# Performance work log

Measured on AMD Instinct MI355X. Metric: run time of the kernel, lower is better.

Reference implementation:

```python
import jax, jax.numpy as jnp
import numpy as np

D, NH, K, FF, S, B = 256, 4, 1024, 1024, 2048, 4  # nhead*d_model must equal key_feature_dim=1024


def _ln(x, g, b, eps=1e-5):
    m = jnp.mean(x, axis=-1, keepdims=True)
    v = jnp.mean((x - m) ** 2, axis=-1, keepdims=True)
    return (x - m) / jnp.sqrt(v + eps) * g + b


def _l2norm(x, eps=1e-12):  # F.normalize(p=2, dim=-1)
    n = jnp.sqrt(jnp.sum(x * x, axis=-1, keepdims=True))
    return x / jnp.maximum(n, eps)


def setup_inputs() -> dict:
    key = jax.random.key(0)
    ks = jax.random.split(key, 16)
    def rn(i, shape, s):
        return jax.random.normal(ks[i], shape, jnp.float32) * jnp.float32(s)
    z = lambda shape: jnp.zeros(shape, jnp.float32)
    o = lambda shape: jnp.ones(shape, jnp.float32)
    return {
        "srcc": jax.random.normal(ks[0], (S, B, D), jnp.float32),
        "memory": jax.random.normal(ks[1], (S, B, D), jnp.float32),
        # per-head RelationUnit weights (stacked over NH heads)
        "WK": rn(2, (NH, K, D), np.sqrt(2.0 / K)),
        "WQ": rn(3, (NH, K, D), np.sqrt(2.0 / K)),
        "WV": rn(4, (NH, D, D), np.sqrt(2.0 / D)),
        "Wt": rn(5, (NH, D, D), np.sqrt(1.0 / D)),   # trans_conv
        # per-head TransNonlinear (extra_nonlinear)
        "e1w": rn(6, (NH, K, D), np.sqrt(1.0 / D)), "e1b": z((NH, K)),
        "e2w": rn(7, (NH, D, K), np.sqrt(1.0 / K)), "e2b": z((NH, D)),
        "eg": o((NH, D)), "eb": z((NH, D)),
        "Wout": rn(8, (D, NH * D), np.sqrt(1.0 / (NH * D))),  # trans_conv_out
        # decoder-layer FFN + norms
        "l1w": rn(9, (FF, D), np.sqrt(1.0 / D)), "l1b": z((FF,)),
        "l2w": rn(10, (D, FF), np.sqrt(1.0 / FF)), "l2b": z((D,)),
        "n1g": o((D,)), "n1b": z((D,)),
        "n3g": o((D,)), "n3b": z((D,)),
    }


def _forward(srcc, memory, WK, WQ, WV, Wt, e1w, e1b, e2w, e2b, eg, eb,
             Wout, l1w, l1b, l2w, l2b, n1g, n1b, n3g, n3b):
    # RMA(query=memory, key=srcc, value=srcc); dropout = identity (eval mode)
    q, kv = memory, srcc  # [S,B,D]
    wk = _l2norm(jnp.einsum('sbd,hkd->hsbk', kv, WK))   # [h,S,B,K]
    wq = _l2norm(jnp.einsum('sbd,hkd->hsbk', q, WQ))
    dot = jnp.einsum('hqbk,hsbk->hbqs', wq, wk)          # [h,B,Sq,Sk]
    aff = jax.nn.softmax(dot, axis=-1)
    # custom renormalization over the *query* axis (torch dim=1 of [B,Sq,Sk])
    aff = aff / (1e-9 + jnp.sum(aff, axis=2, keepdims=True))
    wv = jnp.einsum('sbd,hed->hbse', kv, WV)             # [h,B,Sk,D]
    o = jnp.einsum('hbqs,hbse->hqbe', aff, wv)           # [h,Sq,B,D]
    ru = jax.nn.relu(jnp.einsum('hqbd,hed->hqbe', q[None] - o, Wt))
    # per-head TransNonlinear
    hmid = jax.nn.relu(jnp.einsum('hqbd,hkd->hqbk', ru, e1w) + e1b[:, None, None, :])
    s2 = jnp.einsum('hqbk,hdk->hqbd', hmid, e2w) + e2b[:, None, None, :]
    xh = _ln(ru + s2, eg[:, None, None, :], eb[:, None, None, :])  # [h,S,B,D]
    cat = jnp.moveaxis(xh, 0, 2).reshape(q.shape[0], q.shape[1], NH * D)  # concat heads
    rma_out = jnp.einsum('sbk,dk->sbd', cat, Wout)       # [S,B,D]
    # decoder layer: note the faithful `[0]` indexing from the source
    srcc2 = rma_out[0]                                    # [B,D]
    x = _ln(memory + srcc2[None, :, :], n1g, n1b)         # broadcast residual
    ff = jax.nn.relu(x @ l1w.T + l1b) @ l2w.T + l2b
    return _ln(x + ff, n3g, n3b)


def reference(srcc, memory, WK, WQ, WV, Wt, e1w, e1b, e2w, e2b, eg, eb,
              Wout, l1w, l1b, l2w, l2b, n1g, n1b, n3g, n3b):
    return _forward(srcc, memory, WK, WQ, WV, Wt, e1w, e1b, e2w, e2b, eg, eb,
                    Wout, l1w, l1b, l2w, l2b, n1g, n1b, n3g, n3b)
```

## Files before the change

### kernel.cpp

```cpp
#include <hip/hip_runtime.h>
#include <stdint.h>
#include <stdio.h>

#define S_  2048
#define B_  4
#define D_  256
#define NH_ 4
#define K_  1024
#define FF_ 1024
#define M_  (S_*B_)
#define HB_ (NH_*B_)

#define LDSROW 136
#define PROW 144

typedef float  f32x4  __attribute__((ext_vector_type(4)));
typedef float  f32x2  __attribute__((ext_vector_type(2)));
typedef __bf16 bf16x8 __attribute__((ext_vector_type(8)));

__device__ __forceinline__ float bf2f(unsigned short u) {
  union { unsigned int i; float f; } v; v.i = ((unsigned int)u) << 16; return v.f;
}
__device__ __forceinline__ unsigned short f2bf(float f) {
  union { float f; unsigned int i; } v; v.f = f;
  unsigned int r = v.i + 0x7fffu + ((v.i >> 16) & 1u);
  return (unsigned short)(r >> 16);
}
__device__ __forceinline__ unsigned char f2fp8(float f) {
  return (unsigned char)(__builtin_amdgcn_cvt_pk_fp8_f32(f, f, 0, false) & 0xff);
}

__device__ __forceinline__ int kperm(int k) {
  int ks = k >> 5, quad = (k >> 3) & 3, b = k & 7;
  return ((ks >> 1) << 6) + (quad << 4) + ((ks & 1) << 3) + b;
}

__device__ __forceinline__ void gld_lds16(const void* g, void* l) {
  __builtin_amdgcn_global_load_lds(
      (__attribute__((address_space(1))) void*)(uintptr_t)g,
      (__attribute__((address_space(3))) void*)(uintptr_t)l, 16, 0, 0);
}

__device__ __forceinline__ void gemm_kloop(
    const unsigned short* __restrict__ Ag, const unsigned short* __restrict__ Bg,
    int lda, int ldb, int kdim,
    unsigned short* __restrict__ smA, unsigned short* __restrict__ smB,
    f32x4 acc[4][4])
{
  const int t    = threadIdx.x;
  const int wave = t >> 6;
  const int lane = t & 63;
  const int wm   = (wave >> 1) << 6;
  const int wn   = (wave & 1) << 6;
  const int c16  = lane & 15;
  const int quad = lane >> 4;

  for (int kc = 0; kc < kdim; kc += 64) {
    __syncthreads();
#pragma unroll
    for (int it = 0; it < 4; ++it) {
      int c   = it*256 + t;
      int row = c >> 3;
      int g   = (c & 7) ^ (row & 7);
      const unsigned short* ga = Ag + (size_t)row*lda + kc + g*8;
      const unsigned short* gb = Bg + (size_t)row*ldb + kc + g*8;
      unsigned short* la = smA + (size_t)(it*256 + wave*64)*8;
      unsigned short* lb = smB + (size_t)(it*256 + wave*64)*8;
      gld_lds16(ga, la);
      gld_lds16(gb, lb);
    }
    asm volatile("s_waitcnt vmcnt(0)" ::: "memory");
    __syncthreads();
#pragma unroll
    for (int ks = 0; ks < 2; ++ks) {
      bf16x8 av[4], bv[4];
#pragma unroll
      for (int i = 0; i < 4; ++i) {
        int ra = wm + i*16 + c16;
        av[i] = *(const bf16x8*)(smA + ra*64 + (((ks*4 + quad) ^ (ra & 7)))*8);
        int rb = wn + i*16 + c16;
        bv[i] = *(const bf16x8*)(smB + rb*64 + (((ks*4 + quad) ^ (rb & 7)))*8);
      }
#pragma unroll
      for (int i = 0; i < 4; ++i)
#pragma unroll
        for (int j = 0; j < 4; ++j)
          acc[i][j] = __builtin_amdgcn_mfma_f32_16x16x32_bf16(av[i], bv[j], acc[i][j], 0, 0, 0);
    }
  }
}

__device__ __forceinline__ float blk_sum256(float v, float* red) {
#pragma unroll
  for (int o = 32; o; o >>= 1) v += __shfl_xor(v, o, 64);
  __syncthreads();
  if ((threadIdx.x & 63) == 0) red[threadIdx.x >> 6] = v;
  __syncthreads();
  return red[0] + red[1] + red[2] + red[3];
}

__device__ __forceinline__ float wave_red(float a) {
#pragma unroll
  for (int o = 1; o < 64; o <<= 1) a += __shfl_xor(a, o, 64);
  return a;
}

__global__ void __launch_bounds__(256) k_cvt6z(
    const float* __restrict__ s0, unsigned short* __restrict__ d0,
    const float* __restrict__ s1, unsigned short* __restrict__ d1,
    const float* __restrict__ s2, unsigned short* __restrict__ d2,
    const float* __restrict__ s3, unsigned short* __restrict__ d3,
    const float* __restrict__ s4, unsigned short* __restrict__ d4,
    const float* __restrict__ s5, unsigned short* __restrict__ d5,
    float* __restrict__ zbase, int zfloats) {
  int b = blockIdx.x;
  if (b >= 6656) {
    int i = ((b - 6656)*256 + threadIdx.x)*4;
    if (i + 3 < zfloats) *(float4*)(zbase + i) = float4{0.f,0.f,0.f,0.f};
    return;
  }
  const float* src; unsigned short* dst; int base;
  if      (b < 2048) { src = s0; dst = d0; base = b; }
  else if (b < 4096) { src = s1; dst = d1; base = b - 2048; }
  else if (b < 5120) { src = s2; dst = d2; base = b - 4096; }
  else if (b < 6144) { src = s3; dst = d3; base = b - 5120; }
  else if (b < 6400) { src = s4; dst = d4; base = b - 6144; }
  else               { src = s5; dst = d5; base = b - 6400; }
  int i = (base*256 + threadIdx.x)*4;
  float4 v = *(const float4*)(src + i);
  ushort4 o;
  o.x = f2bf(v.x); o.y = f2bf(v.y); o.z = f2bf(v.z); o.w = f2bf(v.w);
  *(ushort4*)(dst + i) = o;
}

__global__ void __launch_bounds__(256) k_proj2(
    const unsigned short* __restrict__ X0, const unsigned short* __restrict__ W0,
    float* __restrict__ n0p, unsigned char* __restrict__ o0p,
    const unsigned short* __restrict__ X1, const unsigned short* __restrict__ W1,
    float* __restrict__ n1p, unsigned char* __restrict__ o1p) {
  __shared__ __align__(16) unsigned char smbuf[32768];
  unsigned short* sm = (unsigned short*)smbuf;
  int which = blockIdx.x >> 11;
  const unsigned short* X = which ? X1 : X0;
  const unsigned short* W = which ? W1 : W0;
  float* nsq = which ? n1p : n0p;
  unsigned char* outp = which ? o1p : o0p;
  int l = blockIdx.x & 2047, x = l & 7, rblk = l >> 3;
  int m0 = (rblk >> 2)*128;
  int n0 = (x*4 + (rblk & 3))*128;
  f32x4 acc[4][4];
#pragma unroll
  for (int i = 0; i < 4; ++i)
#pragma unroll
    for (int j = 0; j < 4; ++j) acc[i][j] = f32x4{0.f,0.f,0.f,0.f};
  gemm_kloop(X + (size_t)m0*D_, W + (size_t)n0*D_, D_, D_, D_, sm, sm + 128*64, acc);
  const int t = threadIdx.x, wave = t>>6, lane = t&63;
  const int wm = (wave>>1)*64, wn = (wave&1)*64, quad = lane>>4, c16 = lane&15;
  const int h = n0 >> 10;
  unsigned char* sm8 = smbuf;
  __syncthreads();
#pragma unroll
  for (int i = 0; i < 4; ++i)
#pragma unroll
    for (int r = 0; r < 4; ++r) {
      int mloc = wm + i*16 + quad*4 + r;
      float sq = 0.f;
#pragma unroll
      for (int j = 0; j < 4; ++j) {
        float v = acc[i][j][r];
        sm8[mloc*PROW + kperm(wn + j*16 + c16)] = f2fp8(v);
        sq += v*v;
      }
      sq += __shfl_xor(sq, 1, 64); sq += __shfl_xor(sq, 2, 64);
      sq += __shfl_xor(sq, 4, 64); sq += __shfl_xor(sq, 8, 64);
      if (c16 == 0) {
        int m = m0 + mloc;
        atomicAdd(&nsq[(size_t)(h*B_ + (m & 3))*S_ + (m >> 2)], sq);
      }
    }
  __syncthreads();
  const int cg = t & 7, rsub = t >> 3;
#pragma unroll
  for (int c = 0; c < 4; ++c) {
    int mloc = c*32 + rsub;
    int m = m0 + mloc, s = m >> 2, b = m & 3;
    uint4 val = *(const uint4*)(sm8 + mloc*PROW + cg*16);
    *(uint4*)(outp + ((size_t)(h*B_ + b)*S_ + s)*K_ + (n0 & (K_-1)) + cg*16) = val;
  }
}

__global__ void __launch_bounds__(256) k_qkA(const unsigned char* __restrict__ wqa,
    const unsigned char* __restrict__ wka, const float* __restrict__ nq,
    const float* __restrict__ nk, float* __restrict__ lrow,
    unsigned char* __restrict__ E) {
  __shared__ __align__(16) unsigned char smbuf[32768];
  unsigned char* smA = smbuf;
  unsigned char* smB = smA + 128*128;
  int l = blockIdx.x, x = l & 7, rblk = l >> 3;
  int hb = x*2 + (rblk >> 8);
  int r2 = rblk & 255;
  int s0 = (r2 >> 4)*128;
  int q0 = (r2 & 15)*128;
  const unsigned char* A  = wqa + (size_t)hb*S_*K_ + (size_t)q0*K_;
  const unsigned char* Bm = wka + (size_t)hb*S_*K_ + (size_t)s0*K_;
  const int t = threadIdx.x, wave = t>>6, lane = t&63;
  const int wm = (wave>>1)*64, wn = (wave&1)*64, quad = lane>>4, c16 = lane&15;
  f32x4 acc[4][4];
#pragma unroll
  for (int i = 0; i < 4; ++i)
#pragma unroll
    for (int j = 0; j < 4; ++j) acc[i][j] = f32x4{0.f,0.f,0.f,0.f};

  for (int kc = 0; kc < K_; kc += 128) {
    __syncthreads();
#pragma unroll
    for (int it = 0; it < 4; ++it) {
      int c   = it*256 + t;
      int row = c >> 3;
      int g   = (c & 7) ^ (row & 7);
      gld_lds16(A  + (size_t)row*K_ + kc + g*16, smA + (size_t)(it*256 + wave*64)*16);
      gld_lds16(Bm + (size_t)row*K_ + kc + g*16, smB + (size_t)(it*256 + wave*64)*16);
    }
    asm volatile("s_waitcnt vmcnt(0)" ::: "memory");
    __syncthreads();
#pragma unroll
    for (int j2 = 0; j2 < 2; ++j2) {
      uint4 a4[4], b4[4];
#pragma unroll
      for (int i = 0; i < 4; ++i) {
        int ra = wm + i*16 + c16;
        a4[i] = *(const uint4*)(smA + ra*128 + (((j2*4 + quad) ^ (ra & 7)))*16);
        int rb = wn + i*16 + c16;
        b4[i] = *(const uint4*)(smB + rb*128 + (((j2*4 + quad) ^ (rb & 7)))*16);
      }
#pragma unroll
      for (int hh = 0; hh < 2; ++hh)
#pragma unroll
        for (int i = 0; i < 4; ++i)
#pragma unroll
          for (int j = 0; j < 4; ++j)
            acc[i][j] = __builtin_amdgcn_mfma_f32_16x16x32_fp8_fp8(
                ((const long*)&a4[i])[hh], ((const long*)&b4[j])[hh],
                acc[i][j], 0, 0, 0);
    }
  }

  float rk4[4];
#pragma unroll
  for (int j = 0; j < 4; ++j)
    rk4[j] = rsqrtf(nk[(size_t)hb*S_ + s0 + wn + j*16 + c16]);
  unsigned char* sm8 = smbuf;
  __syncthreads();
#pragma unroll
  for (int i = 0; i < 4; ++i)
#pragma unroll
    for (int r = 0; r < 4; ++r) {
      int qloc = wm + i*16 + quad*4 + r;
      float rq = rsqrtf(nq[(size_t)hb*S_ + q0 + qloc]);
      float rs = 0.f;
#pragma unroll
      for (int j = 0; j < 4; ++j) {
        float e = __expf(acc[i][j][r] * rq * rk4[j]);
        rs += e;
        sm8[qloc*PROW + wn + j*16 + c16] = f2fp8(e);
      }
      rs += __shfl_xor(rs, 1, 64); rs += __shfl_xor(rs, 2, 64);
      rs += __shfl_xor(rs, 4, 64); rs += __shfl_xor(rs, 8, 64);
      if (c16 == 0) atomicAdd(&lrow[(size_t)hb*S_ + q0 + qloc], rs);
    }
  __syncthreads();
  const int cg = t & 7, rsub = t >> 3;
#pragma unroll
  for (int c = 0; c < 4; ++c) {
    int qloc = c*32 + rsub;
    uint4 val = *(const uint4*)(sm8 + qloc*PROW + cg*16);
    *(uint4*)(E + ((size_t)hb*S_ + qloc + q0)*S_ + s0 + cg*16) = val;
  }
}

__global__ void __launch_bounds__(256) k_colsumE(const unsigned char* __restrict__ E,
    const float* __restrict__ lrow, float* __restrict__ colsum,
    float* __restrict__ p0) {
  __shared__ float il[128];
  int hb = blockIdx.x, qc = blockIdx.y;
  int t  = threadIdx.x;
  if (t < 128) il[t] = 1.f / lrow[(size_t)hb*S_ + qc*128 + t];
  __syncthreads();
  const unsigned char* Eb = E + (size_t)hb*S_*S_ + (size_t)(qc*128)*S_ + t*8;
  float acc8[8] = {0,0,0,0,0,0,0,0};
  for (int qi = 0; qi < 128; ++qi) {
    uint2 u = *(const uint2*)(Eb + (size_t)qi*S_);
    float w = il[qi];
    f32x2 v01 = __builtin_amdgcn_cvt_pk_f32_fp8(u.x, false);
    f32x2 v23 = __builtin_amdgcn_cvt_pk_f32_fp8(u.x, true);
    f32x2 v45 = __builtin_amdgcn_cvt_pk_f32_fp8(u.y, false);
    f32x2 v67 = __builtin_amdgcn_cvt_pk_f32_fp8(u.y, true);
    float v8[8] = {v01.x, v01.y, v23.x, v23.y, v45.x, v45.y, v67.x, v67.y};
#pragma unroll
    for (int k = 0; k < 8; ++k) acc8[k] += v8[k] * w;
    if (qc == 0 && qi == 0) {
#pragma unroll
      for (int k = 0; k < 8; ++k) p0[(size_t)hb*S_ + t*8 + k] = v8[k] * w;
    }
  }
#pragma unroll
  for (int k = 0; k < 8; ++k)
    atomicAdd(&colsum[(size_t)hb*S_ + t*8 + k], acc8[k]);
}

__global__ void __launch_bounds__(256) k_mid0(const float* __restrict__ p0,
    const float* __restrict__ colsum, const float* __restrict__ kv,
    float* __restrict__ cbuf) {
  __shared__ float aff[128];
  int hb = blockIdx.x, sc = blockIdx.y;
  int b = hb & 3;
  int t = threadIdx.x;
  if (t < 128) {
    int s = sc*128 + t;
    aff[t] = p0[(size_t)hb*S_ + s] / (1e-9f + colsum[(size_t)hb*S_ + s]);
  }
  __syncthreads();
  float acc = 0.f;
#pragma unroll 4
  for (int i = 0; i < 128; ++i) {
    int s = sc*128 + i;
    acc += aff[i] * kv[((size_t)s*B_ + b)*D_ + t];
  }
  atomicAdd(&cbuf[hb*D_ + t], acc);
}

__global__ void __launch_bounds__(256) k_mid1a(const float* __restrict__ cbuf,
    const float* __restrict__ mem, const float* __restrict__ WV,
    const float* __restrict__ Wt, float* __restrict__ ruW) {
  __shared__ float cS[D_], qmo[D_];
  int hb = blockIdx.x, h = hb >> 2, b = hb & 3;
  int t = threadIdx.x, wave = t >> 6, lane = t & 63;
  cS[t] = cbuf[hb*D_ + t];
  __syncthreads();
  float4 cv = *(const float4*)(cS + lane*4);
  for (int rr = 0; rr < 64; ++rr) {
    int e = wave*64 + rr;
    float4 w = *(const float4*)(WV + ((size_t)h*D_ + e)*D_ + lane*4);
    float a = wave_red(cv.x*w.x + cv.y*w.y + cv.z*w.z + cv.w*w.w);
    if (lane == 0) qmo[e] = mem[(size_t)b*D_ + e] - a;
  }
  __syncthreads();
  float4 qv = *(const float4*)(qmo + lane*4);
  for (int rr = 0; rr < 64; ++rr) {
    int e = wave*64 + rr;
    float4 w = *(const float4*)(Wt + ((size_t)h*D_ + e)*D_ + lane*4);
    float a = wave_red(qv.x*w.x + qv.y*w.y + qv.z*w.z + qv.w*w.w);
    if (lane == 0) ruW[hb*D_ + e] = fmaxf(a, 0.f);
  }
}

__global__ void __launch_bounds__(256) k_mid1b(const float* __restrict__ ruW,
    const float* __restrict__ e1w, const float* __restrict__ e1b,
    float* __restrict__ hmW) {
  __shared__ float ru[D_];
  int hb = blockIdx.x, kc = blockIdx.y, h = hb >> 2;
  int t = threadIdx.x, wave = t >> 6, lane = t & 63;
  ru[t] = ruW[hb*D_ + t];
  __syncthreads();
  float4 rv = *(const float4*)(ru + lane*4);
  for (int rr = 0; rr < 32; ++rr) {
    int k = kc*128 + wave*32 + rr;
    float4 w = *(const float4*)(e1w + ((size_t)h*K_ + k)*D_ + lane*4);
    float a = wave_red(rv.x*w.x + rv.y*w.y + rv.z*w.z + rv.w*w.w);
    if (lane == 0) hmW[hb*K_ + k] = fmaxf(a + e1b[(size_t)h*K_ + k], 0.f);
  }
}

__global__ void __launch_bounds__(256) k_mid1c(const float* __restrict__ hmW,
    const float* __restrict__ e2w, const float* __restrict__ e2b,
    float* __restrict__ s2W) {
  __shared__ float hm[K_];
  int hb = blockIdx.x, dc = blockIdx.y, h = hb >> 2;
  int t = threadIdx.x, wave = t >> 6, lane = t & 63;
  for (int k = t; k < K_; k += 256) hm[k] = hmW[hb*K_ + k];
  __syncthreads();
  for (int rr = 0; rr < 8; ++rr) {
    int d = dc*32 + wave*8 + rr;
    const float* row = e2w + ((size_t)h*D_ + d)*K_;
    float a = 0.f;
#pragma unroll
    for (int p = 0; p < 4; ++p) {
      float4 w = *(const float4*)(row + (p*64 + lane)*4);
      float4 hv = *(const float4*)(hm + (p*64 + lane)*4);
      a += w.x*hv.x + w.y*hv.y + w.z*hv.z + w.w*hv.w;
    }
    a = wave_red(a);
    if (lane == 0) s2W[hb*D_ + d] = a + e2b[(size_t)h*D_ + d];
  }
}

__global__ void __launch_bounds__(256) k_mid1d(const float* __restrict__ ruW,
    const float* __restrict__ s2W, const float* __restrict__ eg,
    const float* __restrict__ ebias, float* __restrict__ xh0) {
  __shared__ float red[4];
  int hb = blockIdx.x, h = hb >> 2;
  int t = threadIdx.x;
  float tv = ruW[hb*D_ + t] + s2W[hb*D_ + t];
  float mean = blk_sum256(tv, red) * (1.f/D_);
  float dv = tv - mean;
  float var = blk_sum256(dv*dv, red) * (1.f/D_);
  xh0[hb*D_ + t] = dv * rsqrtf(var + 1e-5f) * eg[(size_t)h*D_ + t] + ebias[(size_t)h*D_ + t];
}

__global__ void __launch_bounds__(256) k_mid2(const float* __restrict__ xh0,
    const float* __restrict__ Wout, float* __restrict__ srcc2) {
  __shared__ float cat[NH_*D_];
  int b = blockIdx.x, dc = blockIdx.y;
  int t = threadIdx.x, wave = t >> 6, lane = t & 63;
  for (int n = t; n < NH_*D_; n += 256)
    cat[n] = xh0[((size_t)(n >> 8)*B_ + b)*D_ + (n & 255)];
  __syncthreads();
  for (int rr = 0; rr < 8; ++rr) {
    int d = dc*32 + wave*8 + rr;
    const float* row = Wout + (size_t)d*(NH_*D_);
    float a = 0.f;
#pragma unroll
    for (int p = 0; p < 4; ++p) {
      float4 w = *(const float4*)(row + (p*64 + lane)*4);
      float4 cv = *(const float4*)(cat + (p*64 + lane)*4);
      a += w.x*cv.x + w.y*cv.y + w.z*cv.z + w.w*cv.w;
    }
    a = wave_red(a);
    if (lane == 0) srcc2[b*D_ + d] = a;
  }
}

__global__ void __launch_bounds__(256) k_f1(const float* __restrict__ mem,
    const float* __restrict__ srcc2, const float* __restrict__ g,
    const float* __restrict__ bb, float* __restrict__ xf,
    unsigned short* __restrict__ xb) {
  __shared__ float red[4];
  int m = blockIdx.x, t = threadIdx.x;
  float v = mem[(size_t)m*D_ + t] + srcc2[(m & 3)*D_ + t];
  float mean = blk_sum256(v, red) * (1.f/D_);
  float d = v - mean;
  float var = blk_sum256(d*d, red) * (1.f/D_);
  float y = d * rsqrtf(var + 1e-5f) * g[t] + bb[t];
  xf[(size_t)m*D_ + t] = y;
  xb[(size_t)m*D_ + t] = f2bf(y);
}

__global__ void __launch_bounds__(256) k_f2(const unsigned short* __restrict__ xb,
    const unsigned short* __restrict__ l1wb, const float* __restrict__ l1b,
    unsigned short* __restrict__ h1) {
  __shared__ __align__(16) unsigned short sm[128*LDSROW];
  int l = blockIdx.x;
  int n0 = (l & 7)*128, m0 = (l >> 3)*128;
  f32x4 acc[4][4];
#pragma unroll
  for (int i = 0; i < 4; ++i)
#pragma unroll
    for (int j = 0; j < 4; ++j) acc[i][j] = f32x4{0.f,0.f,0.f,0.f};
  gemm_kloop(xb + (size_t)m0*D_, l1wb + (size_t)n0*D_, D_, D_, D_, sm, sm + 128*64, acc);
  const int t = threadIdx.x, wave = t>>6, lane = t&63;
  const int wm = (wave>>1)*64, wn = (wave&1)*64, quad = lane>>4, c16 = lane&15;
  __syncthreads();
#pragma unroll
  for (int i = 0; i < 4; ++i)
#pragma unroll
    for (int r = 0; r < 4; ++r) {
      int mloc = wm + i*16 + quad*4 + r;
#pragma unroll
      for (int j = 0; j < 4; ++j) {
        int n = n0 + wn + j*16 + c16;
        sm[mloc*LDSROW + wn + j*16 + c16] = f2bf(fmaxf(acc[i][j][r] + l1b[n], 0.f));
      }
    }
  __syncthreads();
  const int col8 = (t & 15)*8, rsub = t >> 4;
#pragma unroll
  for (int c = 0; c < 8; ++c) {
    int mloc = c*16 + rsub;
    uint4 val = *(const uint4*)(sm + mloc*LDSROW + col8);
    *(uint4*)(h1 + (size_t)(m0 + mloc)*FF_ + n0 + col8) = val;
  }
}

__global__ void __launch_bounds__(256) k_f3(const unsigned short* __restrict__ h1,
    const unsigned short* __restrict__ l2wb, float* __restrict__ y0,
    float* __restrict__ y1, float* __restrict__ y2, float* __restrict__ y3) {
  __shared__ __align__(16) unsigned short smA[128*64], smB[128*64];
  int l = blockIdx.x;
  int z = l & 3, n0 = ((l >> 2) & 1)*128, m0 = (l >> 3)*128;
  float* dst = (z == 0) ? y0 : (z == 1) ? y1 : (z == 2) ? y2 : y3;
  f32x4 acc[4][4];
#pragma unroll
  for (int i = 0; i < 4; ++i)
#pragma unroll
    for (int j = 0; j < 4; ++j) acc[i][j] = f32x4{0.f,0.f,0.f,0.f};
  gemm_kloop(h1 + (size_t)m0*FF_ + z*256, l2wb + (size_t)n0*FF_ + z*256,
             FF_, FF_, 256, smA, smB, acc);
  const int t = threadIdx.x, wave = t>>6, lane = t&63;
  const int wm = (wave>>1)*64, wn = (wave&1)*64, quad = lane>>4, c16 = lane&15;
#pragma unroll
  for (int i = 0; i < 4; ++i)
#pragma unroll
    for (int r = 0; r < 4; ++r) {
      int m = m0 + wm + i*16 + quad*4 + r;
#pragma unroll
      for (int j = 0; j < 4; ++j) {
        int n = n0 + wn + j*16 + c16;
        dst[(size_t)m*D_ + n] = acc[i][j][r];
      }
    }
}

__global__ void __launch_bounds__(256) k_f4(const float* __restrict__ y0,
    const float* __restrict__ y1, const float* __restrict__ y2,
    const float* __restrict__ y3, const float* __restrict__ l2b,
    const float* __restrict__ xf, const float* __restrict__ g,
    const float* __restrict__ bb, float* __restrict__ out) {
  __shared__ float red[4];
  int m = blockIdx.x, t = threadIdx.x;
  size_t idx = (size_t)m*D_ + t;
  float v = y0[idx] + y1[idx] + y2[idx] + y3[idx] + l2b[t] + xf[idx];
  float mean = blk_sum256(v, red) * (1.f/D_);
  float d = v - mean;
  float var = blk_sum256(d*d, red) * (1.f/D_);
  out[idx] = d * rsqrtf(var + 1e-5f) * g[t] + bb[t];
}

constexpr size_t SZ_ACT  = (size_t)HB_*S_*K_;
constexpr size_t OFF_WQA = 0;
constexpr size_t OFF_WKA = OFF_WQA + SZ_ACT;
constexpr size_t OFF_KVB = OFF_WKA + SZ_ACT;
constexpr size_t OFF_QB  = OFF_KVB + (size_t)M_*D_*2;
constexpr size_t OFF_WKW = OFF_QB  + (size_t)M_*D_*2;
constexpr size_t OFF_WQW = OFF_WKW + (size_t)NH_*K_*D_*2;
constexpr size_t OFF_L1W = OFF_WQW + (size_t)NH_*K_*D_*2;
constexpr size_t OFF_L2W = OFF_L1W + (size_t)FF_*D_*2;
constexpr size_t OFF_XB  = OFF_L2W + (size_t)D_*FF_*2;
constexpr size_t OFF_H1  = OFF_XB  + (size_t)M_*D_*2;
constexpr size_t OFF_XF  = OFF_H1  + (size_t)M_*FF_*2;
constexpr size_t OFF_YF0 = OFF_XF  + (size_t)M_*D_*4;
constexpr size_t OFF_YF1 = OFF_YF0 + (size_t)M_*D_*4;
constexpr size_t OFF_YF2 = OFF_YF1 + (size_t)M_*D_*4;
constexpr size_t OFF_YF3 = OFF_YF2 + (size_t)M_*D_*4;
constexpr size_t OFF_NQ  = OFF_YF3 + (size_t)M_*D_*4;
constexpr size_t OFF_NK  = OFF_NQ + (size_t)HB_*S_*4;
constexpr size_t OFF_L   = OFF_NK + (size_t)HB_*S_*4;
constexpr size_t OFF_CS  = OFF_L  + (size_t)HB_*S_*4;
constexpr size_t OFF_CB  = OFF_CS + (size_t)HB_*S_*4;
constexpr size_t ZERO_BYTES = (size_t)HB_*S_*4*4 + (size_t)HB_*D_*4;
constexpr size_t OFF_P0  = OFF_CB + (size_t)HB_*D_*4;
constexpr size_t OFF_XH0 = OFF_P0 + (size_t)HB_*S_*4;
constexpr size_t OFF_SC2 = OFF_XH0 + (size_t)HB_*D_*4;
constexpr size_t OFF_RU  = OFF_SC2 + (size_t)B_*D_*4;
constexpr size_t OFF_HM  = OFF_RU  + (size_t)HB_*D_*4;
constexpr size_t OFF_S2  = OFF_HM  + (size_t)HB_*K_*4;
constexpr size_t OFF_E   = OFF_S2  + (size_t)HB_*D_*4;
constexpr size_t SZ_E    = (size_t)HB_*S_*S_;
constexpr size_t NEED_ALL = OFF_E + SZ_E;

extern "C" void kernel_launch(void* const* d_in, const int* in_sizes, int n_in,
                              void* d_out, int out_size, void* d_ws, size_t ws_size,
                              hipStream_t stream) {
  (void)in_sizes; (void)out_size;
  if (n_in < 21) return;
  const float* srcc = (const float*)d_in[0];
  const float* mem  = (const float*)d_in[1];
  const float* WK   = (const float*)d_in[2];
  const float* WQ   = (const float*)d_in[3];
  const float* WV   = (const float*)d_in[4];
  const float* Wt   = (const float*)d_in[5];
  const float* e1w  = (const float*)d_in[6];
  const float* e1b  = (const float*)d_in[7];
  const float* e2w  = (const float*)d_in[8];
  const float* e2b  = (const float*)d_in[9];
  const float* eg   = (const float*)d_in[10];
  const float* eb   = (const float*)d_in[11];
  const float* Wout = (const float*)d_in[12];
  const float* l1w  = (const float*)d_in[13];
  const float* l1b  = (const float*)d_in[14];
  const float* l2w  = (const float*)d_in[15];
  const float* l2b  = (const float*)d_in[16];
  const float* n1g  = (const float*)d_in[17];
  const float* n1b  = (const float*)d_in[18];
  const float* n3g  = (const float*)d_in[19];
  const float* n3b  = (const float*)d_in[20];

  char* ws = (char*)d_ws;
  if (ws_size < NEED_ALL) {
    fprintf(stderr, "kernel_launch: ws_size=%zu < required %zu bytes — aborting\n",
            ws_size, NEED_ALL);
    return;
  }

  unsigned char*  wqa  = (unsigned char*)(ws + OFF_WQA);
  unsigned char*  wka  = (unsigned char*)(ws + OFF_WKA);
  unsigned short* kvb  = (unsigned short*)(ws + OFF_KVB);
  unsigned short* qb   = (unsigned short*)(ws + OFF_QB);
  unsigned short* wkw  = (unsigned short*)(ws + OFF_WKW);
  unsigned short* wqw  = (unsigned short*)(ws + OFF_WQW);
  unsigned short* l1wb = (unsigned short*)(ws + OFF_L1W);
  unsigned short* l2wb = (unsigned short*)(ws + OFF_L2W);
  unsigned short* xb   = (unsigned short*)(ws + OFF_XB);
  unsigned short* h1   = (unsigned short*)(ws + OFF_H1);
  float* xf    = (float*)(ws + OFF_XF);
  float* yf0   = (float*)(ws + OFF_YF0);
  float* yf1   = (float*)(ws + OFF_YF1);
  float* yf2   = (float*)(ws + OFF_YF2);
  float* yf3   = (float*)(ws + OFF_YF3);
  float* nq    = (float*)(ws + OFF_NQ);
  float* nk    = (float*)(ws + OFF_NK);
  float* lrow  = (float*)(ws + OFF_L);
  float* cs    = (float*)(ws + OFF_CS);
  float* cbuf  = (float*)(ws + OFF_CB);
  float* p0    = (float*)(ws + OFF_P0);
  float* xh0   = (float*)(ws + OFF_XH0);
  float* sc2   = (float*)(ws + OFF_SC2);
  float* ruW   = (float*)(ws + OFF_RU);
  float* hmW   = (float*)(ws + OFF_HM);
  float* s2W   = (float*)(ws + OFF_S2);
  unsigned char* E = (unsigned char*)(ws + OFF_E);

  int zfloats = (int)(ZERO_BYTES/4);
  int zblocks = (zfloats + 1023)/1024;
  k_cvt6z<<<6656 + zblocks, 256, 0, stream>>>(srcc, kvb, mem, qb, WK, wkw,
                                              WQ, wqw, l1w, l1wb, l2w, l2wb,
                                              nq, zfloats);

  k_proj2<<<4096, 256, 0, stream>>>(kvb, wkw, nk, wka, qb, wqw, nq, wqa);

  k_qkA<<<4096, 256, 0, stream>>>(wqa, wka, nq, nk, lrow, E);
  k_colsumE<<<dim3(HB_, 16), 256, 0, stream>>>(E, lrow, cs, p0);

  k_mid0<<<dim3(HB_, S_/128), 256, 0, stream>>>(p0, cs, srcc, cbuf);
  k_mid1a<<<HB_, 256, 0, stream>>>(cbuf, mem, WV, Wt, ruW);
  k_mid1b<<<dim3(HB_, 8), 256, 0, stream>>>(ruW, e1w, e1b, hmW);
  k_mid1c<<<dim3(HB_, 8), 256, 0, stream>>>(hmW, e2w, e2b, s2W);
  k_mid1d<<<HB_, 256, 0, stream>>>(ruW, s2W, eg, eb, xh0);
  k_mid2<<<dim3(B_, 8), 256, 0, stream>>>(xh0, Wout, sc2);

  k_f1<<<M_, 256, 0, stream>>>(mem, sc2, n1g, n1b, xf, xb);
  k_f2<<<512, 256, 0, stream>>>(xb, l1wb, l1b, h1);
  k_f3<<<512, 256, 0, stream>>>(h1, l2wb, yf0, yf1, yf2, yf3);
  k_f4<<<M_, 256, 0, stream>>>(yf0, yf1, yf2, yf3, l2b, xf, n3g, n3b,
                               (float*)d_out);
}
```

Before: 604.9 us.

## Run Q/K projection GEMM in FP8 and halve split-K in final FFN GEMM

The input activations and the WK/WQ weights are converted to FP8 (with a K-permuted layout) instead of bf16, and the projection GEMM uses a shared FP8 MFMA k-loop that is also reused by the QK kernel. This halves the conversion and GEMM load bytes and doubles MFMA throughput for the projections. The risk is lower precision in the projections, which feed L2-normalisation and softmax. Separately, the second FFN GEMM's split-K drops from 4 to 2, so half as many fp32 partial buffers are written and read in the final LayerNorm, at the cost of fewer blocks.

```diff
diff --git a/kernel.cpp b/kernel.cpp
--- a/kernel.cpp
+++ b/kernel.cpp
@@ -62,12 +62,8 @@
       int c   = it*256 + t;
       int row = c >> 3;
       int g   = (c & 7) ^ (row & 7);
-      const unsigned short* ga = Ag + (size_t)row*lda + kc + g*8;
-      const unsigned short* gb = Bg + (size_t)row*ldb + kc + g*8;
-      unsigned short* la = smA + (size_t)(it*256 + wave*64)*8;
-      unsigned short* lb = smB + (size_t)(it*256 + wave*64)*8;
-      gld_lds16(ga, la);
-      gld_lds16(gb, lb);
+      gld_lds16(Ag + (size_t)row*lda + kc + g*8, smA + (size_t)(it*256 + wave*64)*8);
+      gld_lds16(Bg + (size_t)row*ldb + kc + g*8, smB + (size_t)(it*256 + wave*64)*8);
     }
     asm volatile("s_waitcnt vmcnt(0)" ::: "memory");
     __syncthreads();
@@ -90,6 +86,55 @@
   }
 }
 
+__device__ __forceinline__ void gemm_kloop_fp8(
+    const unsigned char* __restrict__ Ag, const unsigned char* __restrict__ Bg,
+    int lda, int ldb, int kdim,
+    unsigned char* __restrict__ smA, unsigned char* __restrict__ smB,
+    f32x4 acc[4][4])
+{
+  const int t    = threadIdx.x;
+  const int wave = t >> 6;
+  const int lane = t & 63;
+  const int wm   = (wave >> 1) << 6;
+  const int wn   = (wave & 1) << 6;
+  const int c16  = lane & 15;
+  const int quad = lane >> 4;
+
+  for (int kc = 0; kc < kdim; kc += 128) {
+    __syncthreads();
+#pragma unroll
+    for (int it = 0; it < 4; ++it) {
+      int c   = it*256 + t;
+      int row = c >> 3;
+      int g   = (c & 7) ^ (row & 7);
+      gld_lds16(Ag + (size_t)row*lda + kc + g*16, smA + (size_t)(it*256 + wave*64)*16);
+      gld_lds16(Bg + (size_t)row*ldb + kc + g*16, smB + (size_t)(it*256 + wave*64)*16);
+    }
+    asm volatile("s_waitcnt vmcnt(0)" ::: "memory");
+    __syncthreads();
+#pragma unroll
+    for (int j2 = 0; j2 < 2; ++j2) {
+      uint4 a4[4], b4[4];
+#pragma unroll
+      for (int i = 0; i < 4; ++i) {
+        int ra = wm + i*16 + c16;
+        a4[i] = *(const uint4*)(smA + ra*128 + (((j2*4 + quad) ^ (ra & 7)))*16);
+        int rb = wn + i*16 + c16;
+        b4[i] = *(const uint4*)(smB + rb*128 + (((j2*4 + quad) ^ (rb & 7)))*16);
+      }
+#pragma unroll
+      for (int hh = 0; hh < 2; ++hh)
+#pragma unroll
+        for (int i = 0; i < 4; ++i)
+#pragma unroll
+          for (int j = 0; j < 4; ++j)
+            acc[i][j] = __builtin_amdgcn_mfma_f32_16x16x32_fp8_fp8(
+                ((const long*)&a4[i])[hh], ((const long*)&b4[j])[hh],
+                acc[i][j], 0, 0, 0);
+    }
+  }
+}
+
 __device__ __forceinline__ float blk_sum256(float v, float* red) {
 #pragma unroll
   for (int o = 32; o; o >>= 1) v += __shfl_xor(v, o, 64);
@@ -105,11 +150,11 @@
   return a;
 }
 
-__global__ void __launch_bounds__(256) k_cvt6z(
-    const float* __restrict__ s0, unsigned short* __restrict__ d0,
-    const float* __restrict__ s1, unsigned short* __restrict__ d1,
-    const float* __restrict__ s2, unsigned short* __restrict__ d2,
-    const float* __restrict__ s3, unsigned short* __restrict__ d3,
+__global__ void __launch_bounds__(256) k_cvtmix(
+    const float* __restrict__ s0, unsigned char* __restrict__ d0,
+    const float* __restrict__ s1, unsigned char* __restrict__ d1,
+    const float* __restrict__ s2, unsigned char* __restrict__ d2,
+    const float* __restrict__ s3, unsigned char* __restrict__ d3,
     const float* __restrict__ s4, unsigned short* __restrict__ d4,
     const float* __restrict__ s5, unsigned short* __restrict__ d5,
     float* __restrict__ zbase, int zfloats) {
@@ -119,30 +164,41 @@
     if (i + 3 < zfloats) *(float4*)(zbase + i) = float4{0.f,0.f,0.f,0.f};
     return;
   }
-  const float* src; unsigned short* dst; int base;
+  if (b >= 6144) {
+    const float* src; unsigned short* dst; int base;
+    if (b < 6400) { src = s4; dst = d4; base = b - 6144; }
+    else          { src = s5; dst = d5; base = b - 6400; }
+    int i = (base*256 + threadIdx.x)*4;
+    float4 v = *(const float4*)(src + i);
+    ushort4 o;
+    o.x = f2bf(v.x); o.y = f2bf(v.y); o.z = f2bf(v.z); o.w = f2bf(v.w);
+    *(ushort4*)(dst + i) = o;
+    return;
+  }
+  const float* src; unsigned char* dst; int base;
   if      (b < 2048) { src = s0; dst = d0; base = b; }
   else if (b < 4096) { src = s1; dst = d1; base = b - 2048; }
   else if (b < 5120) { src = s2; dst = d2; base = b - 4096; }
-  else if (b < 6144) { src = s3; dst = d3; base = b - 5120; }
-  else if (b < 6400) { src = s4; dst = d4; base = b - 6144; }
-  else               { src = s5; dst = d5; base = b - 6400; }
+  else               { src = s3; dst = d3; base = b - 5120; }
   int i = (base*256 + threadIdx.x)*4;
   float4 v = *(const float4*)(src + i);
-  ushort4 o;
-  o.x = f2bf(v.x); o.y = f2bf(v.y); o.z = f2bf(v.z); o.w = f2bf(v.w);
-  *(ushort4*)(dst + i) = o;
+  uchar4 o;
+  o.x = f2fp8(v.x); o.y = f2fp8(v.y); o.z = f2fp8(v.z); o.w = f2fp8(v.w);
+  int dsto = (i & ~127) + kperm(i & 127);
+  *(uchar4*)(dst + dsto) = o;
 }
 
 __global__ void __launch_bounds__(256) k_proj2(
-    const unsigned short* __restrict__ X0, const unsigned short* __restrict__ W0,
+    const unsigned char* __restrict__ X0, const unsigned char* __restrict__ W0,
     float* __restrict__ n0p, unsigned char* __restrict__ o0p,
-    const unsigned short* __restrict__ X1, const unsigned short* __restrict__ W1,
+    const unsigned char* __restrict__ X1, const unsigned char* __restrict__ W1,
     float* __restrict__ n1p, unsigned char* __restrict__ o1p) {
   __shared__ __align__(16) unsigned char smbuf[32768];
-  unsigned short* sm = (unsigned short*)smbuf;
+  unsigned char* smA = smbuf;
+  unsigned char* smB = smbuf + 16384;
   int which = blockIdx.x >> 11;
-  const unsigned short* X = which ? X1 : X0;
-  const unsigned short* W = which ? W1 : W0;
+  const unsigned char* X = which ? X1 : X0;
+  const unsigned char* W = which ? W1 : W0;
   float* nsq = which ? n1p : n0p;
   unsigned char* outp = which ? o1p : o0p;
   int l = blockIdx.x & 2047, x = l & 7, rblk = l >> 3;
@@ -153,7 +209,7 @@
   for (int i = 0; i < 4; ++i)
 #pragma unroll
     for (int j = 0; j < 4; ++j) acc[i][j] = f32x4{0.f,0.f,0.f,0.f};
-  gemm_kloop(X + (size_t)m0*D_, W + (size_t)n0*D_, D_, D_, D_, sm, sm + 128*64, acc);
+  gemm_kloop_fp8(X + (size_t)m0*D_, W + (size_t)n0*D_, D_, D_, D_, smA, smB, acc);
   const int t = threadIdx.x, wave = t>>6, lane = t&63;
   const int wm = (wave>>1)*64, wn = (wave&1)*64, quad = lane>>4, c16 = lane&15;
   const int h = n0 >> 10;
@@ -195,7 +251,7 @@
     unsigned char* __restrict__ E) {
   __shared__ __align__(16) unsigned char smbuf[32768];
   unsigned char* smA = smbuf;
-  unsigned char* smB = smA + 128*128;
+  unsigned char* smB = smbuf + 16384;
   int l = blockIdx.x, x = l & 7, rblk = l >> 3;
   int hb = x*2 + (rblk >> 8);
   int r2 = rblk & 255;
@@ -210,40 +266,7 @@
   for (int i = 0; i < 4; ++i)
 #pragma unroll
     for (int j = 0; j < 4; ++j) acc[i][j] = f32x4{0.f,0.f,0.f,0.f};
-
-  for (int kc = 0; kc < K_; kc += 128) {
-    __syncthreads();
-#pragma unroll
-    for (int it = 0; it < 4; ++it) {
-      int c   = it*256 + t;
-      int row = c >> 3;
-      int g   = (c & 7) ^ (row & 7);
-      gld_lds16(A  + (size_t)row*K_ + kc + g*16, smA + (size_t)(it*256 + wave*64)*16);
-      gld_lds16(Bm + (size_t)row*K_ + kc + g*16, smB + (size_t)(it*256 + wave*64)*16);
-    }
-    asm volatile("s_waitcnt vmcnt(0)" ::: "memory");
-    __syncthreads();
-#pragma unroll
-    for (int j2 = 0; j2 < 2; ++j2) {
-      uint4 a4[4], b4[4];
-#pragma unroll
-      for (int i = 0; i < 4; ++i) {
-        int ra = wm + i*16 + c16;
-        a4[i] = *(const uint4*)(smA + ra*128 + (((j2*4 + quad) ^ (ra & 7)))*16);
-        int rb = wn + i*16 + c16;
-        b4[i] = *(const uint4*)(smB + rb*128 + (((j2*4 + quad) ^ (rb & 7)))*16);
-      }
-#pragma unroll
-      for (int hh = 0; hh < 2; ++hh)
-#pragma unroll
-        for (int i = 0; i < 4; ++i)
-#pragma unroll
-          for (int j = 0; j < 4; ++j)
-            acc[i][j] = __builtin_amdgcn_mfma_f32_16x16x32_fp8_fp8(
-                ((const long*)&a4[i])[hh], ((const long*)&b4[j])[hh],
-                acc[i][j], 0, 0, 0);
-    }
-  }
+  gemm_kloop_fp8(A, Bm, K_, K_, K_, smA, smB, acc);
 
   float rk4[4];
 #pragma unroll
@@ -274,7 +297,7 @@
   for (int c = 0; c < 4; ++c) {
     int qloc = c*32 + rsub;
     uint4 val = *(const uint4*)(sm8 + qloc*PROW + cg*16);
-    *(uint4*)(E + ((size_t)hb*S_ + qloc + q0)*S_ + s0 + cg*16) = val;
+    *(uint4*)(E + ((size_t)hb*S_ + q0 + qloc)*S_ + s0 + cg*16) = val;
   }
 }
 
@@ -482,19 +505,19 @@
 }
 
 __global__ void __launch_bounds__(256) k_f3(const unsigned short* __restrict__ h1,
-    const unsigned short* __restrict__ l2wb, float* __restrict__ y0,
-    float* __restrict__ y1, float* __restrict__ y2, float* __restrict__ y3) {
+    const unsigned short* __restrict__ l2wb, float* __restrict__ yfa,
+    float* __restrict__ yfb) {
   __shared__ __align__(16) unsigned short smA[128*64], smB[128*64];
   int l = blockIdx.x;
-  int z = l & 3, n0 = ((l >> 2) & 1)*128, m0 = (l >> 3)*128;
-  float* dst = (z == 0) ? y0 : (z == 1) ? y1 : (z == 2) ? y2 : y3;
+  int z = l & 1, n0 = ((l >> 1) & 1)*128, m0 = (l >> 2)*128;
+  float* dst = z ? yfb : yfa;
   f32x4 acc[4][4];
 #pragma unroll
   for (int i = 0; i < 4; ++i)
 #pragma unroll
     for (int j = 0; j < 4; ++j) acc[i][j] = f32x4{0.f,0.f,0.f,0.f};
-  gemm_kloop(h1 + (size_t)m0*FF_ + z*256, l2wb + (size_t)n0*FF_ + z*256,
-             FF_, FF_, 256, smA, smB, acc);
+  gemm_kloop(h1 + (size_t)m0*FF_ + z*512, l2wb + (size_t)n0*FF_ + z*512,
+             FF_, FF_, 512, smA, smB, acc);
   const int t = threadIdx.x, wave = t>>6, lane = t&63;
   const int wm = (wave>>1)*64, wn = (wave&1)*64, quad = lane>>4, c16 = lane&15;
 #pragma unroll
@@ -510,15 +533,14 @@
     }
 }
 
-__global__ void __launch_bounds__(256) k_f4(const float* __restrict__ y0,
-    const float* __restrict__ y1, const float* __restrict__ y2,
-    const float* __restrict__ y3, const float* __restrict__ l2b,
+__global__ void __launch_bounds__(256) k_f4(const float* __restrict__ yfa,
+    const float* __restrict__ yfb, const float* __restrict__ l2b,
     const float* __restrict__ xf, const float* __restrict__ g,
     const float* __restrict__ bb, float* __restrict__ out) {
   __shared__ float red[4];
   int m = blockIdx.x, t = threadIdx.x;
   size_t idx = (size_t)m*D_ + t;
-  float v = y0[idx] + y1[idx] + y2[idx] + y3[idx] + l2b[t] + xf[idx];
+  float v = yfa[idx] + yfb[idx] + l2b[t] + xf[idx];
   float mean = blk_sum256(v, red) * (1.f/D_);
   float d = v - mean;
   float var = blk_sum256(d*d, red) * (1.f/D_);
@@ -529,19 +551,17 @@
 constexpr size_t OFF_WQA = 0;
 constexpr size_t OFF_WKA = OFF_WQA + SZ_ACT;
 constexpr size_t OFF_KVB = OFF_WKA + SZ_ACT;
-constexpr size_t OFF_QB  = OFF_KVB + (size_t)M_*D_*2;
-constexpr size_t OFF_WKW = OFF_QB  + (size_t)M_*D_*2;
-constexpr size_t OFF_WQW = OFF_WKW + (size_t)NH_*K_*D_*2;
-constexpr size_t OFF_L1W = OFF_WQW + (size_t)NH_*K_*D_*2;
+constexpr size_t OFF_QB  = OFF_KVB + (size_t)M_*D_;
+constexpr size_t OFF_WKW = OFF_QB  + (size_t)M_*D_;
+constexpr size_t OFF_WQW = OFF_WKW + (size_t)NH_*K_*D_;
+constexpr size_t OFF_L1W = OFF_WQW + (size_t)NH_*K_*D_;
 constexpr size_t OFF_L2W = OFF_L1W + (size_t)FF_*D_*2;
 constexpr size_t OFF_XB  = OFF_L2W + (size_t)D_*FF_*2;
 constexpr size_t OFF_H1  = OFF_XB  + (size_t)M_*D_*2;
 constexpr size_t OFF_XF  = OFF_H1  + (size_t)M_*FF_*2;
 constexpr size_t OFF_YF0 = OFF_XF  + (size_t)M_*D_*4;
 constexpr size_t OFF_YF1 = OFF_YF0 + (size_t)M_*D_*4;
-constexpr size_t OFF_YF2 = OFF_YF1 + (size_t)M_*D_*4;
-constexpr size_t OFF_YF3 = OFF_YF2 + (size_t)M_*D_*4;
-constexpr size_t OFF_NQ  = OFF_YF3 + (size_t)M_*D_*4;
+constexpr size_t OFF_NQ  = OFF_YF1 + (size_t)M_*D_*4;
 constexpr size_t OFF_NK  = OFF_NQ + (size_t)HB_*S_*4;
 constexpr size_t OFF_L   = OFF_NK + (size_t)HB_*S_*4;
 constexpr size_t OFF_CS  = OFF_L  + (size_t)HB_*S_*4;
@@ -593,10 +613,10 @@
 
   unsigned char*  wqa  = (unsigned char*)(ws + OFF_WQA);
   unsigned char*  wka  = (unsigned char*)(ws + OFF_WKA);
-  unsigned short* kvb  = (unsigned short*)(ws + OFF_KVB);
-  unsigned short* qb   = (unsigned short*)(ws + OFF_QB);
-  unsigned short* wkw  = (unsigned short*)(ws + OFF_WKW);
-  unsigned short* wqw  = (unsigned short*)(ws + OFF_WQW);
+  unsigned char*  kvb8 = (unsigned char*)(ws + OFF_KVB);
+  unsigned char*  qb8  = (unsigned char*)(ws + OFF_QB);
+  unsigned char*  wkw8 = (unsigned char*)(ws + OFF_WKW);
+  unsigned char*  wqw8 = (unsigned char*)(ws + OFF_WQW);
   unsigned short* l1wb = (unsigned short*)(ws + OFF_L1W);
   unsigned short* l2wb = (unsigned short*)(ws + OFF_L2W);
   unsigned short* xb   = (unsigned short*)(ws + OFF_XB);
@@ -604,8 +624,6 @@
   float* xf    = (float*)(ws + OFF_XF);
   float* yf0   = (float*)(ws + OFF_YF0);
   float* yf1   = (float*)(ws + OFF_YF1);
-  float* yf2   = (float*)(ws + OFF_YF2);
-  float* yf3   = (float*)(ws + OFF_YF3);
   float* nq    = (float*)(ws + OFF_NQ);
   float* nk    = (float*)(ws + OFF_NK);
   float* lrow  = (float*)(ws + OFF_L);
@@ -621,11 +639,11 @@
 
   int zfloats = (int)(ZERO_BYTES/4);
   int zblocks = (zfloats + 1023)/1024;
-  k_cvt6z<<<6656 + zblocks, 256, 0, stream>>>(srcc, kvb, mem, qb, WK, wkw,
-                                              WQ, wqw, l1w, l1wb, l2w, l2wb,
-                                              nq, zfloats);
-
-  k_proj2<<<4096, 256, 0, stream>>>(kvb, wkw, nk, wka, qb, wqw, nq, wqa);
+  k_cvtmix<<<6656 + zblocks, 256, 0, stream>>>(srcc, kvb8, mem, qb8, WK, wkw8,
+                                               WQ, wqw8, l1w, l1wb, l2w, l2wb,
+                                               nq, zfloats);
+
+  k_proj2<<<4096, 256, 0, stream>>>(kvb8, wkw8, nk, wka, qb8, wqw8, nq, wqa);
 
   k_qkA<<<4096, 256, 0, stream>>>(wqa, wka, nq, nk, lrow, E);
   k_colsumE<<<dim3(HB_, 16), 256, 0, stream>>>(E, lrow, cs, p0);
@@ -639,7 +657,6 @@
 
   k_f1<<<M_, 256, 0, stream>>>(mem, sc2, n1g, n1b, xf, xb);
   k_f2<<<512, 256, 0, stream>>>(xb, l1wb, l1b, h1);
-  k_f3<<<512, 256, 0, stream>>>(h1, l2wb, yf0, yf1, yf2, yf3);
-  k_f4<<<M_, 256, 0, stream>>>(yf0, yf1, yf2, yf3, l2b, xf, n3g, n3b,
-                               (float*)d_out);
-}
+  k_f3<<<256, 256, 0, stream>>>(h1, l2wb, yf0, yf1);
+  k_f4<<<M_, 256, 0, stream>>>(yf0, yf1, l2b, xf, n3g, n3b, (float*)d_out);
+}
```

After: 562.2 us (median of 2 runs). 1.08x faster.
